# Performance work log

Measured on AMD Instinct MI355X. Metric: run time of the kernel, lower is better.

## Reference

```python
import jax, jax.numpy as jnp
import numpy as np

D = 256; FF = 1024; NH = 8; NL = 4; NP = 4; DH = D // NH
SHAPES = [(64, 64), (32, 32), (16, 16), (8, 8)]
B = 4; N = sum(h * w for h, w in SHAPES)


def _ln(x, g, b, eps=1e-5):
    m = jnp.mean(x, -1, keepdims=True)
    v = jnp.var(x, -1, keepdims=True)
    return (x - m) * jax.lax.rsqrt(v + eps) * g + b


def _bilinear(v, x, y, H, W):
    # v: [B, H*W, nh, dh]; x, y: [B, Nq, nh, P] pixel coords (grid_sample, align_corners=False, zero pad)
    x0 = jnp.floor(x); y0 = jnp.floor(y)
    fx = x - x0; fy = y - y0
    x0 = x0.astype(jnp.int32); y0 = y0.astype(jnp.int32)
    dh = v.shape[-1]
    acc = 0.0
    for xi, yi, w in ((x0, y0, (1 - fx) * (1 - fy)),
                      (x0 + 1, y0, fx * (1 - fy)),
                      (x0, y0 + 1, (1 - fx) * fy),
                      (x0 + 1, y0 + 1, fx * fy)):
        valid = ((xi >= 0) & (xi < W) & (yi >= 0) & (yi < H)).astype(v.dtype)
        idx = jnp.clip(yi, 0, H - 1) * W + jnp.clip(xi, 0, W - 1)  # [B,Nq,nh,P]
        Bq, Nq, nh, P = idx.shape
        idx2 = idx.transpose(0, 1, 3, 2).reshape(Bq, Nq * P, nh, 1)
        idx2 = jnp.broadcast_to(idx2, (Bq, Nq * P, nh, dh))
        g = jnp.take_along_axis(v, idx2, axis=1)  # [B, Nq*P, nh, dh]
        g = g.reshape(Bq, Nq, P, nh, dh).transpose(0, 1, 3, 2, 4)  # [B,Nq,nh,P,dh]
        acc = acc + g * (w * valid)[..., None]
    return acc


def _msdeform(value, loc, attn, shapes):
    # value [B,N,nh,dh]; loc [B,Nq,nh,L,P,2] in [0,1]; attn [B,Nq,nh,L,P]
    out = 0.0; start = 0
    for l, (H, W) in enumerate(shapes):
        v = value[:, start:start + H * W]
        start += H * W
        x = loc[:, :, :, l, :, 0] * W - 0.5
        y = loc[:, :, :, l, :, 1] * H - 0.5
        s = _bilinear(v, x, y, H, W)  # [B,Nq,nh,P,dh]
        out = out + jnp.einsum('bqhpd,bqhp->bqhd', s, attn[:, :, :, l, :])
    return out


def _forward(src, pos, reference_points, w_value, b_value, w_off, b_off, w_attn, b_attn,
             w_out, b_out, g1, be1, w1, b1, w2, b2, g2, be2, padding_mask, shapes):
    q = src + pos
    value = src @ w_value.T + b_value
    value = jnp.where(padding_mask[..., None], 0.0, value).reshape(B, N, NH, DH)
    off = (q @ w_off.T + b_off).reshape(B, N, NH, NL, NP, 2)
    attn = jax.nn.softmax((q @ w_attn.T + b_attn).reshape(B, N, NH, NL * NP), axis=-1)
    attn = attn.reshape(B, N, NH, NL, NP)
    normalizer = jnp.array([[w, h] for h, w in shapes], jnp.float32)  # [L,2] as (W,H)
    loc = reference_points[:, :, None, :, None, :] + off / normalizer[None, None, None, :, None, :]
    a = _msdeform(value, loc, attn, shapes).reshape(B, N, D) @ w_out.T + b_out
    x = _ln(src + a, g1, be1)
    f = jax.nn.relu(x @ w1.T + b1) @ w2.T + b2
    return _ln(x + f, g2, be2)


def setup_inputs() -> dict:
    key = jax.random.key(0)
    ks = iter(jax.random.split(key, 24))
    def p(shape, scale=0.02):
        return jax.random.normal(next(ks), shape, jnp.float32) * scale
    d = {}
    d['src'] = jax.random.normal(next(ks), (B, N, D), jnp.float32)
    d['pos'] = jax.random.normal(next(ks), (B, N, D), jnp.float32)
    d['reference_points'] = jax.random.uniform(next(ks), (B, N, NL, 2), dtype=jnp.float32)
    d['w_value'] = p((D, D)); d['b_value'] = jnp.zeros((D,), jnp.float32)
    d['w_off'] = p((NH * NL * NP * 2, D), 0.001); d['b_off'] = p((NH * NL * NP * 2,), 0.1)
    d['w_attn'] = p((NH * NL * NP, D)); d['b_attn'] = jnp.zeros((NH * NL * NP,), jnp.float32)
    d['w_out'] = p((D, D)); d['b_out'] = jnp.zeros((D,), jnp.float32)
    d['g1'] = jnp.ones((D,), jnp.float32); d['be1'] = jnp.zeros((D,), jnp.float32)
    d['w1'] = p((FF, D)); d['b1'] = jnp.zeros((FF,), jnp.float32)
    d['w2'] = p((D, FF)); d['b2'] = jnp.zeros((D,), jnp.float32)
    d['g2'] = jnp.ones((D,), jnp.float32); d['be2'] = jnp.zeros((D,), jnp.float32)
    d['spatial_shapes'] = jnp.array(SHAPES, jnp.int32)
    d['level_start_index'] = jnp.array(np.cumsum([0] + [h * w for h, w in SHAPES[:-1]]), jnp.int32)
    d['padding_mask'] = jnp.zeros((B, N), bool)
    return d


def reference(src, pos, reference_points, w_value, b_value, w_off, b_off, w_attn, b_attn,
              w_out, b_out, g1, be1, w1, b1, w2, b2, g2, be2,
              spatial_shapes, level_start_index, padding_mask):
    shapes = [tuple(map(int, s)) for s in np.asarray(spatial_shapes)]  # static per-level shapes
    return _forward(src, pos, reference_points, w_value, b_value, w_off, b_off, w_attn, b_attn,
                    w_out, b_out, g1, be1, w1, b1, w2, b2, g2, be2, padding_mask, shapes)
```

## Files before the change

kernel.cpp:

```cpp
#include <hip/hip_runtime.h>

#define B_SZ   4
#define NTOK   5440
#define MTOT   (B_SZ*NTOK)
#define DMODEL 256
#define FFDIM  1024

typedef __attribute__((ext_vector_type(8))) __bf16 bf16x8;
typedef __attribute__((ext_vector_type(4))) float  f32x4;

static __device__ __forceinline__ unsigned short f2b(float f) {
    unsigned u = __builtin_bit_cast(unsigned, f);
    u = (u + 0x7FFF + ((u >> 16) & 1)) >> 16;
    return (unsigned short)u;
}
static __device__ __forceinline__ float b2f(unsigned short s) {
    return __builtin_bit_cast(float, (unsigned)s << 16);
}
static __device__ __forceinline__ float lo_bf(unsigned u) {
    return __builtin_bit_cast(float, u << 16);
}
static __device__ __forceinline__ float hi_bf(unsigned u) {
    return __builtin_bit_cast(float, u & 0xffff0000u);
}

#define GLL(gp, lp) __builtin_amdgcn_global_load_lds( \
    (const __attribute__((address_space(1))) void*)(gp), \
    (__attribute__((address_space(3))) void*)(lp), 16, 0, 0)

__global__ __launch_bounds__(256)
void qkv_gemm(const unsigned short* __restrict__ src_bf,
              const unsigned short* __restrict__ q_bf,
              const unsigned short* __restrict__ wv_b,
              const unsigned short* __restrict__ woa_b,
              const float* __restrict__ b_value,
              const float* __restrict__ b_off, const float* __restrict__ b_attn,
              const unsigned char* __restrict__ rowmask,
              unsigned short* __restrict__ value_b, unsigned short* __restrict__ oa_b)
{
    const int K = 256;
    const int y = blockIdx.x;
    const bool isv = (y < 2);
    const unsigned short* A  = isv ? src_bf : q_bf;
    const unsigned short* Wt = isv ? wv_b : woa_b;
    unsigned short* C = isv ? value_b : oa_b;
    const int ldc  = isv ? 256 : 384;
    const int col0 = (isv ? y : (y - 2)) * 128;

    __shared__ unsigned short As[128 * 32];
    __shared__ unsigned short Bs[128 * 32];
    const int tid  = threadIdx.x;
    const int lane = tid & 63;
    const int wave = tid >> 6;
    const int row0 = blockIdx.y * 128;
    const int wr = (wave >> 1) * 64, wc = (wave & 1) * 64;
    const int mrow = lane & 15, quad = lane >> 4;

    f32x4 acc[4][4] = {};
    const int ri0 = tid >> 2,            ki0 = (tid & 3) * 8;
    const int ri1 = (256 + tid) >> 2,    ki1 = ((256 + tid) & 3) * 8;
    const int lds0 = (wave * 64) * 8, lds1 = (256 + wave * 64) * 8;

    for (int k0 = 0; k0 < K; k0 += 32) {
        __syncthreads();
        GLL(A  + (size_t)(row0 + ri0) * K + k0 + ki0, &As[lds0]);
        GLL(Wt + (size_t)(col0 + ri0) * K + k0 + ki0, &Bs[lds0]);
        GLL(A  + (size_t)(row0 + ri1) * K + k0 + ki1, &As[lds1]);
        GLL(Wt + (size_t)(col0 + ri1) * K + k0 + ki1, &Bs[lds1]);
        __syncthreads();

        bf16x8 af[4], bfr[4];
        #pragma unroll
        for (int t4 = 0; t4 < 4; ++t4) {
            af[t4]  = *(const bf16x8*)&As[(wr + t4 * 16 + mrow) * 32 + quad * 8];
            bfr[t4] = *(const bf16x8*)&Bs[(wc + t4 * 16 + mrow) * 32 + quad * 8];
        }
        #pragma unroll
        for (int ti = 0; ti < 4; ++ti)
            #pragma unroll
            for (int tj = 0; tj < 4; ++tj)
                acc[ti][tj] = __builtin_amdgcn_mfma_f32_16x16x32_bf16(
                                  af[ti], bfr[tj], acc[ti][tj], 0, 0, 0);
    }

    #pragma unroll
    for (int tj = 0; tj < 4; ++tj) {
        const int col = col0 + wc + tj * 16 + mrow;
        const float bv = isv ? b_value[col] : (col < 256 ? b_off[col] : b_attn[col - 256]);
        #pragma unroll
        for (int ti = 0; ti < 4; ++ti)
            #pragma unroll
            for (int r = 0; r < 4; ++r) {
                const int row = row0 + wr + ti * 16 + quad * 4 + r;
                float v = acc[ti][tj][r] + bv;
                if (isv && rowmask[row]) v = 0.f;
                C[(size_t)row * ldc + col] = f2b(v);
            }
    }
}

__global__ __launch_bounds__(256)
void mfma_gemm(const unsigned short* __restrict__ A,
               const unsigned short* __restrict__ Wt,
               const float* __restrict__ bias,
               unsigned short* __restrict__ Cb,
               int M, int Nout, int K, int relu)
{
    __shared__ unsigned short As[128 * 32];
    __shared__ unsigned short Bs[128 * 32];
    const int tid  = threadIdx.x;
    const int lane = tid & 63;
    const int wave = tid >> 6;
    const int row0 = blockIdx.y * 128, col0 = blockIdx.x * 128;
    const int wr = (wave >> 1) * 64, wc = (wave & 1) * 64;
    const int mrow = lane & 15, quad = lane >> 4;

    f32x4 acc[4][4] = {};
    const int ri0 = tid >> 2,            ki0 = (tid & 3) * 8;
    const int ri1 = (256 + tid) >> 2,    ki1 = ((256 + tid) & 3) * 8;
    const int lds0 = (wave * 64) * 8, lds1 = (256 + wave * 64) * 8;

    for (int k0 = 0; k0 < K; k0 += 32) {
        __syncthreads();
        GLL(A  + (size_t)(row0 + ri0) * K + k0 + ki0, &As[lds0]);
        GLL(Wt + (size_t)(col0 + ri0) * K + k0 + ki0, &Bs[lds0]);
        GLL(A  + (size_t)(row0 + ri1) * K + k0 + ki1, &As[lds1]);
        GLL(Wt + (size_t)(col0 + ri1) * K + k0 + ki1, &Bs[lds1]);
        __syncthreads();

        bf16x8 af[4], bfr[4];
        #pragma unroll
        for (int t4 = 0; t4 < 4; ++t4) {
            af[t4]  = *(const bf16x8*)&As[(wr + t4 * 16 + mrow) * 32 + quad * 8];
            bfr[t4] = *(const bf16x8*)&Bs[(wc + t4 * 16 + mrow) * 32 + quad * 8];
        }
        #pragma unroll
        for (int ti = 0; ti < 4; ++ti)
            #pragma unroll
            for (int tj = 0; tj < 4; ++tj)
                acc[ti][tj] = __builtin_amdgcn_mfma_f32_16x16x32_bf16(
                                  af[ti], bfr[tj], acc[ti][tj], 0, 0, 0);
    }

    #pragma unroll
    for (int tj = 0; tj < 4; ++tj) {
        const int col = col0 + wc + tj * 16 + mrow;
        const float bv = bias[col];
        #pragma unroll
        for (int ti = 0; ti < 4; ++ti)
            #pragma unroll
            for (int r = 0; r < 4; ++r) {
                const int row = row0 + wr + ti * 16 + quad * 4 + r;
                float v = acc[ti][tj][r] + bv;
                if (relu) v = fmaxf(v, 0.f);
                Cb[(size_t)row * Nout + col] = f2b(v);
            }
    }
}

__global__ __launch_bounds__(256)
void gemm_ln(const unsigned short* __restrict__ A,
             const unsigned short* __restrict__ Wt,
             const float* __restrict__ bias,
             const float* __restrict__ resid,
             const float* __restrict__ g, const float* __restrict__ be,
             float* __restrict__ out_f, unsigned short* __restrict__ out_b,
             int K)
{
    __shared__ unsigned short As[32 * 32];
    __shared__ unsigned short Bs[256 * 32];
    __shared__ float s_red[32][8];

    const int tid  = threadIdx.x;
    const int lane = tid & 63;
    const int wave = tid >> 6;
    const int row0 = blockIdx.x * 32;
    const int mrow = lane & 15, quad = lane >> 4;
    const int colw = wave * 64;

    f32x4 acc[2][4] = {};
    const int ri = tid >> 2, ki = (tid & 3) * 8;

    for (int k0 = 0; k0 < K; k0 += 32) {
        __syncthreads();
        if (wave < 2)
            GLL(A + (size_t)(row0 + ri) * K + k0 + ki, &As[(wave * 64) * 8]);
        #pragma unroll
        for (int rep = 0; rep < 4; ++rep)
            GLL(Wt + (size_t)(rep * 64 + ri) * K + k0 + ki,
                &Bs[(rep * 256 + wave * 64) * 8]);
        __syncthreads();

        bf16x8 af[2], bfr[4];
        #pragma unroll
        for (int ti = 0; ti < 2; ++ti)
            af[ti] = *(const bf16x8*)&As[(ti * 16 + mrow) * 32 + quad * 8];
        #pragma unroll
        for (int tj = 0; tj < 4; ++tj)
            bfr[tj] = *(const bf16x8*)&Bs[(colw + tj * 16 + mrow) * 32 + quad * 8];
        #pragma unroll
        for (int ti = 0; ti < 2; ++ti)
            #pragma unroll
            for (int tj = 0; tj < 4; ++tj)
                acc[ti][tj] = __builtin_amdgcn_mfma_f32_16x16x32_bf16(
                                  af[ti], bfr[tj], acc[ti][tj], 0, 0, 0);
    }

    float bv[4], gv[4], bev[4];
    #pragma unroll
    for (int tj = 0; tj < 4; ++tj) {
        const int col = colw + tj * 16 + mrow;
        bv[tj] = bias[col]; gv[tj] = g[col]; bev[tj] = be[col];
    }

    #pragma unroll
    for (int ti = 0; ti < 2; ++ti) {
        #pragma unroll
        for (int r = 0; r < 4; ++r) {
            const int row_local = ti * 16 + quad * 4 + r;
            const int row = row0 + row_local;
            float s = 0.f, sq = 0.f;
            #pragma unroll
            for (int tj = 0; tj < 4; ++tj) {
                const int col = colw + tj * 16 + mrow;
                float t = acc[ti][tj][r] + bv[tj] + resid[(size_t)row * 256 + col];
                acc[ti][tj][r] = t;
                s += t; sq += t * t;
            }
            #pragma unroll
            for (int m = 1; m < 16; m <<= 1) {
                s  += __shfl_xor(s, m, 64);
                sq += __shfl_xor(sq, m, 64);
            }
            if (mrow == 0) { s_red[row_local][wave] = s; s_red[row_local][4 + wave] = sq; }
        }
    }
    __syncthreads();

    #pragma unroll
    for (int ti = 0; ti < 2; ++ti) {
        #pragma unroll
        for (int r = 0; r < 4; ++r) {
            const int row_local = ti * 16 + quad * 4 + r;
            const int row = row0 + row_local;
            const float4 su = *(const float4*)&s_red[row_local][0];
            const float4 qu = *(const float4*)&s_red[row_local][4];
            const float mean = (su.x + su.y + su.z + su.w) * (1.f / 256.f);
            const float var  = (qu.x + qu.y + qu.z + qu.w) * (1.f / 256.f) - mean * mean;
            const float rstd = rsqrtf(var + 1e-5f);
            #pragma unroll
            for (int tj = 0; tj < 4; ++tj) {
                const int col = colw + tj * 16 + mrow;
                const float o = (acc[ti][tj][r] - mean) * rstd * gv[tj] + bev[tj];
                out_f[(size_t)row * 256 + col] = o;
                if (out_b) out_b[(size_t)row * 256 + col] = f2b(o);
            }
        }
    }
}

__global__ __launch_bounds__(256)
void sampling_kernel(const unsigned short* __restrict__ value,
                     const unsigned short* __restrict__ oa,
                     const float* __restrict__ refp,
                     unsigned short* __restrict__ samp)
{
    __shared__ unsigned s_pk[64 * 68];
    const int t0  = blockIdx.x * 8;
    const int tid = threadIdx.x;

    #pragma unroll
    for (int rep = 0; rep < 4; ++rep) {
        const int e   = rep * 256 + tid;
        const int tok = e >> 7;
        const int hp  = e & 127;
        const int h   = hp >> 4, i16 = hp & 15, l = i16 >> 2;
        const int t   = t0 + tok;

        const float ex = __expf(b2f(oa[(size_t)t * 384 + 256 + h * 16 + i16]));
        float ssum = ex;
        #pragma unroll
        for (int o = 8; o; o >>= 1) ssum += __shfl_xor(ssum, o, 16);
        const float aw = ex / ssum;

        const int   Wl_t[4]  = {64, 32, 16, 8};
        const int   LST_t[4] = {0, 4096, 5120, 5376};
        const int   Wl  = Wl_t[l];
        const int   LST = LST_t[l];
        const float fW  = (float)Wl;

        const unsigned ov = *(const unsigned*)&oa[(size_t)t * 384 + h * 32 + i16 * 2];
        const float ox = lo_bf(ov), oy = hi_bf(ov);
        const float2 rxy = *(const float2*)&refp[(size_t)t * 8 + l * 2];
        const float x = rxy.x * fW + ox - 0.5f;
        const float y = rxy.y * fW + oy - 0.5f;
        const float x0 = floorf(x), y0 = floorf(y);
        const float fx = x - x0, fy = y - y0;
        const int   ix = (int)x0, iy = (int)y0;
        const bool  vx0 = (ix >= 0) & (ix < Wl), vx1 = (ix + 1 >= 0) & (ix + 1 < Wl);

        const int base = (tok * 8 + h) * 68 + i16 * 4;
        #pragma unroll
        for (int j = 0; j < 2; ++j) {
            const int  yv = iy + j;
            const bool vy = (yv >= 0) & (yv < Wl);
            const float wy = (j ? fy : 1.f - fy) * aw;
            const int  rowi = LST + yv * Wl;
            const float w0 = (vy & vx0) ? wy * (1.f - fx) : 0.f;
            const float w1 = (vy & vx1) ? wy * fx : 0.f;
            const unsigned i0 = (vy & vx0) ? (unsigned)(rowi + ix) : 0u;
            const unsigned i1 = (vy & vx1) ? (unsigned)(rowi + ix + 1) : 0u;
            s_pk[base + j * 2 + 0] = (i0 << 16) | f2b(w0);
            s_pk[base + j * 2 + 1] = (i1 << 16) | f2b(w1);
        }
    }
    __syncthreads();

    const int wv_  = tid >> 6;
    const int lane = tid & 63;
    const int t2   = lane >> 5;
    const int h    = (lane >> 2) & 7;
    const int dq   = lane & 3;
    const int tok  = wv_ * 2 + t2;
    const int t    = t0 + tok;
    const int b    = t / NTOK;
    const char* vb = (const char*)value + ((size_t)b * NTOK * 256 + h * 32 + dq * 8) * 2;
    const unsigned* sp = s_pk + (tok * 8 + h) * 68;

    float a0 = 0.f, a1 = 0.f, a2 = 0.f, a3 = 0.f;
    float a4 = 0.f, a5 = 0.f, a6 = 0.f, a7 = 0.f;

    unsigned pkc = sp[0];
    uint4 vc = *(const uint4*)(vb + (size_t)(pkc >> 16) * 512);
    #pragma unroll 8
    for (int i = 0; i < 64; ++i) {
        unsigned pkn = 0; uint4 vn = make_uint4(0, 0, 0, 0);
        if (i < 63) {
            pkn = sp[i + 1];
            vn = *(const uint4*)(vb + (size_t)(pkn >> 16) * 512);
        }
        const float w = lo_bf(pkc);
        a0 += lo_bf(vc.x) * w; a1 += hi_bf(vc.x) * w;
        a2 += lo_bf(vc.y) * w; a3 += hi_bf(vc.y) * w;
        a4 += lo_bf(vc.z) * w; a5 += hi_bf(vc.z) * w;
        a6 += lo_bf(vc.w) * w; a7 += hi_bf(vc.w) * w;
        pkc = pkn; vc = vn;
    }
    ushort4 o0, o1;
    o0.x = f2b(a0); o0.y = f2b(a1); o0.z = f2b(a2); o0.w = f2b(a3);
    o1.x = f2b(a4); o1.y = f2b(a5); o1.z = f2b(a6); o1.w = f2b(a7);
    unsigned short* op = samp + (size_t)t * 256 + h * 32 + dq * 8;
    *(ushort4*)(op)     = o0;
    *(ushort4*)(op + 4) = o1;
}

__global__ __launch_bounds__(256)
void prep_kernel(const float* __restrict__ src, const float* __restrict__ pos,
                 const float* __restrict__ wv, const float* __restrict__ woff,
                 const float* __restrict__ wattn, const float* __restrict__ wout,
                 const float* __restrict__ w1, const float* __restrict__ w2,
                 unsigned short* __restrict__ q_bf, unsigned short* __restrict__ src_bf,
                 unsigned short* __restrict__ wv_b, unsigned short* __restrict__ woa_b,
                 unsigned short* __restrict__ wout_b,
                 unsigned short* __restrict__ w1_b, unsigned short* __restrict__ w2_b)
{
    const int v = blockIdx.x * 256 + threadIdx.x;
    if (v < 1392640) {
        const float4 s = ((const float4*)src)[v];
        const float4 p = ((const float4*)pos)[v];
        ushort4 qo, so;
        qo.x = f2b(s.x + p.x); qo.y = f2b(s.y + p.y);
        qo.z = f2b(s.z + p.z); qo.w = f2b(s.w + p.w);
        so.x = f2b(s.x); so.y = f2b(s.y); so.z = f2b(s.z); so.w = f2b(s.w);
        ((ushort4*)q_bf)[v]   = qo;
        ((ushort4*)src_bf)[v] = so;
        return;
    }
    const int v2 = v - 1392640;
    const float* s; unsigned short* d; int off;
    if      (v2 <  16384) { s = wv;    d = wv_b;          off = v2; }
    else if (v2 <  32768) { s = woff;  d = woa_b;         off = v2 - 16384; }
    else if (v2 <  40960) { s = wattn; d = woa_b + 65536; off = v2 - 32768; }
    else if (v2 <  57344) { s = wout;  d = wout_b;        off = v2 - 40960; }
    else if (v2 < 122880) { s = w1;    d = w1_b;          off = v2 - 57344; }
    else                  { s = w2;    d = w2_b;          off = v2 - 122880; }
    const float4 f = ((const float4*)s)[off];
    ushort4 u; u.x = f2b(f.x); u.y = f2b(f.y); u.z = f2b(f.z); u.w = f2b(f.w);
    ((ushort4*)d)[off] = u;
}

extern "C" void kernel_launch(void* const* d_in, const int* in_sizes, int n_in,
                              void* d_out, int out_size, void* d_ws, size_t ws_size,
                              hipStream_t stream) {
    const float* src     = (const float*)d_in[0];
    const float* pos     = (const float*)d_in[1];
    const float* refp    = (const float*)d_in[2];
    const float* w_value = (const float*)d_in[3];
    const float* b_value = (const float*)d_in[4];
    const float* w_off   = (const float*)d_in[5];
    const float* b_off   = (const float*)d_in[6];
    const float* w_attn  = (const float*)d_in[7];
    const float* b_attn  = (const float*)d_in[8];
    const float* w_out   = (const float*)d_in[9];
    const float* b_out   = (const float*)d_in[10];
    const float* g1      = (const float*)d_in[11];
    const float* be1     = (const float*)d_in[12];
    const float* w1      = (const float*)d_in[13];
    const float* b1      = (const float*)d_in[14];
    const float* w2      = (const float*)d_in[15];
    const float* b2      = (const float*)d_in[16];
    const float* g2      = (const float*)d_in[17];
    const float* be2     = (const float*)d_in[18];
    const unsigned char* pmask = (const unsigned char*)d_in[21];

    char* ws = (char*)d_ws;
    const size_t SZ16 = (size_t)MTOT * 256 * 2;
    unsigned short* q_bf    = (unsigned short*)(ws);
    unsigned short* src_bf  = (unsigned short*)(ws + SZ16);
    unsigned short* value_b = (unsigned short*)(ws + 2 * SZ16);
    unsigned short* oa_b    = (unsigned short*)(ws + 3 * SZ16);
    unsigned short* samp    = (unsigned short*)(ws + 3 * SZ16 + SZ16 * 3 / 2);
    unsigned short* h_bf    = (unsigned short*)(ws + 5 * SZ16 + SZ16 * 3 / 2);
    unsigned short* wts     = (unsigned short*)(ws + 9 * SZ16 + SZ16 * 3 / 2);
    float*          x       = (float*)(ws);
    unsigned short* x_bf    = (unsigned short*)(ws + 2 * SZ16);

    unsigned short* wv_b    = wts;
    unsigned short* woa_b   = wv_b   + 65536;
    unsigned short* wout_b  = woa_b  + 98304;
    unsigned short* w1_b    = wout_b + 65536;
    unsigned short* w2_b    = w1_b   + 262144;

    const dim3 blk(256);

    prep_kernel<<<dim3(6176), blk, 0, stream>>>(src, pos, w_value, w_off, w_attn,
                                                w_out, w1, w2, q_bf, src_bf,
                                                wv_b, woa_b, wout_b, w1_b, w2_b);
    qkv_gemm<<<dim3(5, MTOT / 128), blk, 0, stream>>>(
        src_bf, q_bf, wv_b, woa_b, b_value, b_off, b_attn, pmask, value_b, oa_b);
    sampling_kernel<<<dim3(MTOT / 8), blk, 0, stream>>>(value_b, oa_b, refp, samp);
    gemm_ln<<<dim3(MTOT / 32), blk, 0, stream>>>(
        samp, wout_b, b_out, src, g1, be1, x, x_bf, DMODEL);
    mfma_gemm<<<dim3(FFDIM / 128, MTOT / 128), blk, 0, stream>>>(
        x_bf, w1_b, b1, h_bf, MTOT, FFDIM, DMODEL, 1);
    gemm_ln<<<dim3(MTOT / 32), blk, 0, stream>>>(
        h_bf, w2_b, b2, x, g2, be2, (float*)d_out, nullptr, FFDIM);
}
```

Measured before the change: 271.5 us.

## Split fused GEMM+LayerNorm into 128x64-tile GEMM and separate add-LayerNorm kernel

Replaces the fused gemm_ln kernel, whose 32x256 tiles reload the full weight tile for only 32 rows, with a 128x64-tile bf16 GEMM plus a separate vectorized residual-add LayerNorm kernel. The aim is better weight reuse per loaded A row and better tile shape for the out-projection and FFN2 GEMMs. In exchange the GEMM output makes an extra bf16 round trip through global memory. The second residual is now read from the bf16 copy of x rather than fp32, and the first GEMM output is rounded to bf16 before LayerNorm, which reduces precision.

```diff
diff --git a/kernel.cpp b/kernel.cpp
--- a/kernel.cpp
+++ b/kernel.cpp
@@ -159,45 +159,41 @@
 }
 
 __global__ __launch_bounds__(256)
-void gemm_ln(const unsigned short* __restrict__ A,
-             const unsigned short* __restrict__ Wt,
-             const float* __restrict__ bias,
-             const float* __restrict__ resid,
-             const float* __restrict__ g, const float* __restrict__ be,
-             float* __restrict__ out_f, unsigned short* __restrict__ out_b,
-             int K)
-{
-    __shared__ unsigned short As[32 * 32];
-    __shared__ unsigned short Bs[256 * 32];
-    __shared__ float s_red[32][8];
-
+void gemm_n64(const unsigned short* __restrict__ A,
+              const unsigned short* __restrict__ Wt,
+              const float* __restrict__ bias,
+              unsigned short* __restrict__ Cb,
+              int M, int Nout, int K)
+{
+    __shared__ unsigned short As[128 * 32];
+    __shared__ unsigned short Bs[64 * 32];
     const int tid  = threadIdx.x;
     const int lane = tid & 63;
     const int wave = tid >> 6;
-    const int row0 = blockIdx.x * 32;
+    const int row0 = blockIdx.y * 128, col0 = blockIdx.x * 64;
+    const int wr = wave * 32;
     const int mrow = lane & 15, quad = lane >> 4;
-    const int colw = wave * 64;
 
     f32x4 acc[2][4] = {};
-    const int ri = tid >> 2, ki = (tid & 3) * 8;
+    const int ri0 = tid >> 2,            ki0 = (tid & 3) * 8;
+    const int ri1 = (256 + tid) >> 2,    ki1 = ((256 + tid) & 3) * 8;
+    const int ldsA0 = (wave * 64) * 8, ldsA1 = (256 + wave * 64) * 8;
+    const int ldsB  = (wave * 64) * 8;
 
     for (int k0 = 0; k0 < K; k0 += 32) {
         __syncthreads();
-        if (wave < 2)
-            GLL(A + (size_t)(row0 + ri) * K + k0 + ki, &As[(wave * 64) * 8]);
-        #pragma unroll
-        for (int rep = 0; rep < 4; ++rep)
-            GLL(Wt + (size_t)(rep * 64 + ri) * K + k0 + ki,
-                &Bs[(rep * 256 + wave * 64) * 8]);
+        GLL(A  + (size_t)(row0 + ri0) * K + k0 + ki0, &As[ldsA0]);
+        GLL(A  + (size_t)(row0 + ri1) * K + k0 + ki1, &As[ldsA1]);
+        GLL(Wt + (size_t)(col0 + ri0) * K + k0 + ki0, &Bs[ldsB]);
         __syncthreads();
 
         bf16x8 af[2], bfr[4];
         #pragma unroll
         for (int ti = 0; ti < 2; ++ti)
-            af[ti] = *(const bf16x8*)&As[(ti * 16 + mrow) * 32 + quad * 8];
+            af[ti] = *(const bf16x8*)&As[(wr + ti * 16 + mrow) * 32 + quad * 8];
         #pragma unroll
         for (int tj = 0; tj < 4; ++tj)
-            bfr[tj] = *(const bf16x8*)&Bs[(colw + tj * 16 + mrow) * 32 + quad * 8];
+            bfr[tj] = *(const bf16x8*)&Bs[(tj * 16 + mrow) * 32 + quad * 8];
         #pragma unroll
         for (int ti = 0; ti < 2; ++ti)
             #pragma unroll
@@ -206,56 +202,65 @@
                                   af[ti], bfr[tj], acc[ti][tj], 0, 0, 0);
     }
 
-    float bv[4], gv[4], bev[4];
     #pragma unroll
     for (int tj = 0; tj < 4; ++tj) {
-        const int col = colw + tj * 16 + mrow;
-        bv[tj] = bias[col]; gv[tj] = g[col]; bev[tj] = be[col];
-    }
-
+        const int col = col0 + tj * 16 + mrow;
+        const float bv = bias[col];
+        #pragma unroll
+        for (int ti = 0; ti < 2; ++ti)
+            #pragma unroll
+            for (int r = 0; r < 4; ++r) {
+                const int row = row0 + wr + ti * 16 + quad * 4 + r;
+                Cb[(size_t)row * Nout + col] = f2b(acc[ti][tj][r] + bv);
+            }
+    }
+}
+
+__global__ __launch_bounds__(256)
+void addln_kernel(const unsigned short* __restrict__ c,
+                  const float* __restrict__ resid_f,
+                  const unsigned short* __restrict__ resid_b,
+                  const float* __restrict__ g, const float* __restrict__ be,
+                  float* __restrict__ out_f, unsigned short* __restrict__ out_b)
+{
+    const int wave = threadIdx.x >> 6;
+    const int lane = threadIdx.x & 63;
+    const int row  = blockIdx.x * 4 + wave;
+    const size_t base = (size_t)row * 256 + (lane << 2);
+
+    const ushort4 cu = *(const ushort4*)(c + base);
+    float4 v;
+    v.x = b2f(cu.x); v.y = b2f(cu.y); v.z = b2f(cu.z); v.w = b2f(cu.w);
+    if (resid_f) {
+        const float4 r = *(const float4*)(resid_f + base);
+        v.x += r.x; v.y += r.y; v.z += r.z; v.w += r.w;
+    } else {
+        const ushort4 r = *(const ushort4*)(resid_b + base);
+        v.x += b2f(r.x); v.y += b2f(r.y); v.z += b2f(r.z); v.w += b2f(r.w);
+    }
+
+    float s  = v.x + v.y + v.z + v.w;
+    float ss = v.x * v.x + v.y * v.y + v.z * v.z + v.w * v.w;
     #pragma unroll
-    for (int ti = 0; ti < 2; ++ti) {
-        #pragma unroll
-        for (int r = 0; r < 4; ++r) {
-            const int row_local = ti * 16 + quad * 4 + r;
-            const int row = row0 + row_local;
-            float s = 0.f, sq = 0.f;
-            #pragma unroll
-            for (int tj = 0; tj < 4; ++tj) {
-                const int col = colw + tj * 16 + mrow;
-                float t = acc[ti][tj][r] + bv[tj] + resid[(size_t)row * 256 + col];
-                acc[ti][tj][r] = t;
-                s += t; sq += t * t;
-            }
-            #pragma unroll
-            for (int m = 1; m < 16; m <<= 1) {
-                s  += __shfl_xor(s, m, 64);
-                sq += __shfl_xor(sq, m, 64);
-            }
-            if (mrow == 0) { s_red[row_local][wave] = s; s_red[row_local][4 + wave] = sq; }
-        }
-    }
-    __syncthreads();
-
-    #pragma unroll
-    for (int ti = 0; ti < 2; ++ti) {
-        #pragma unroll
-        for (int r = 0; r < 4; ++r) {
-            const int row_local = ti * 16 + quad * 4 + r;
-            const int row = row0 + row_local;
-            const float4 su = *(const float4*)&s_red[row_local][0];
-            const float4 qu = *(const float4*)&s_red[row_local][4];
-            const float mean = (su.x + su.y + su.z + su.w) * (1.f / 256.f);
-            const float var  = (qu.x + qu.y + qu.z + qu.w) * (1.f / 256.f) - mean * mean;
-            const float rstd = rsqrtf(var + 1e-5f);
-            #pragma unroll
-            for (int tj = 0; tj < 4; ++tj) {
-                const int col = colw + tj * 16 + mrow;
-                const float o = (acc[ti][tj][r] - mean) * rstd * gv[tj] + bev[tj];
-                out_f[(size_t)row * 256 + col] = o;
-                if (out_b) out_b[(size_t)row * 256 + col] = f2b(o);
-            }
-        }
+    for (int off = 32; off; off >>= 1) {
+        s  += __shfl_xor(s, off, 64);
+        ss += __shfl_xor(ss, off, 64);
+    }
+    const float mean = s * (1.f / 256.f);
+    const float var  = ss * (1.f / 256.f) - mean * mean;
+    const float rstd = rsqrtf(var + 1e-5f);
+
+    const float4 gv = *(const float4*)(g  + (lane << 2));
+    const float4 bv = *(const float4*)(be + (lane << 2));
+    float4 o;
+    o.x = (v.x - mean) * rstd * gv.x + bv.x;
+    o.y = (v.y - mean) * rstd * gv.y + bv.y;
+    o.z = (v.z - mean) * rstd * gv.z + bv.z;
+    o.w = (v.w - mean) * rstd * gv.w + bv.w;
+    if (out_f) *(float4*)(out_f + base) = o;
+    if (out_b) {
+        ushort4 u; u.x = f2b(o.x); u.y = f2b(o.y); u.z = f2b(o.z); u.w = f2b(o.w);
+        *(ushort4*)(out_b + base) = u;
     }
 }
 
@@ -422,8 +427,9 @@
     unsigned short* samp    = (unsigned short*)(ws + 3 * SZ16 + SZ16 * 3 / 2);
     unsigned short* h_bf    = (unsigned short*)(ws + 5 * SZ16 + SZ16 * 3 / 2);
     unsigned short* wts     = (unsigned short*)(ws + 9 * SZ16 + SZ16 * 3 / 2);
-    float*          x       = (float*)(ws);
-    unsigned short* x_bf    = (unsigned short*)(ws + 2 * SZ16);
+    unsigned short* C1_bf   = (unsigned short*)(ws + 2 * SZ16);
+    unsigned short* x_bf    = (unsigned short*)(ws);
+    unsigned short* C2_bf   = samp;
 
     unsigned short* wv_b    = wts;
     unsigned short* woa_b   = wv_b   + 65536;
@@ -439,10 +445,14 @@
     qkv_gemm<<<dim3(5, MTOT / 128), blk, 0, stream>>>(
         src_bf, q_bf, wv_b, woa_b, b_value, b_off, b_attn, pmask, value_b, oa_b);
     sampling_kernel<<<dim3(MTOT / 8), blk, 0, stream>>>(value_b, oa_b, refp, samp);
-    gemm_ln<<<dim3(MTOT / 32), blk, 0, stream>>>(
-        samp, wout_b, b_out, src, g1, be1, x, x_bf, DMODEL);
+    gemm_n64<<<dim3(4, MTOT / 128), blk, 0, stream>>>(
+        samp, wout_b, b_out, C1_bf, MTOT, DMODEL, DMODEL);
+    addln_kernel<<<dim3(MTOT / 4), blk, 0, stream>>>(
+        C1_bf, src, nullptr, g1, be1, nullptr, x_bf);
     mfma_gemm<<<dim3(FFDIM / 128, MTOT / 128), blk, 0, stream>>>(
         x_bf, w1_b, b1, h_bf, MTOT, FFDIM, DMODEL, 1);
-    gemm_ln<<<dim3(MTOT / 32), blk, 0, stream>>>(
-        h_bf, w2_b, b2, x, g2, be2, (float*)d_out, nullptr, FFDIM);
-}
+    gemm_n64<<<dim3(4, MTOT / 128), blk, 0, stream>>>(
+        h_bf, w2_b, b2, C2_bf, MTOT, DMODEL, FFDIM);
+    addln_kernel<<<dim3(MTOT / 4), blk, 0, stream>>>(
+        C2_bf, nullptr, x_bf, g2, be2, (float*)d_out, nullptr);
+}
```

New measurement: 279.4 us. +2.9%, slower.
